# Kernel tuning notes

Hardware: AMD Instinct MI355X
Metric: run time of the kernel (lower is better)

Reference implementation:

```python
import jax, jax.numpy as jnp
import numpy as np

WEIGHT = 1.0

# 3x3x3 discrete Laplacian stencil (6-connected, center -6), as in the torch module
_LAP_K = jnp.array(
    [[[0, 0, 0], [0, 1, 0], [0, 0, 0]],
     [[0, 1, 0], [1, -6, 1], [0, 1, 0]],
     [[0, 0, 0], [0, 1, 0], [0, 0, 0]]], dtype=jnp.float32)


def _abs_laplacian3d(x):
    """x: (N, D, H, W) -> |3D Laplacian(x)| with zero padding, same shape."""
    y = jax.lax.conv_general_dilated(
        x[:, None],              # (N, 1, D, H, W)
        _LAP_K[None, None],      # (1, 1, 3, 3, 3)
        window_strides=(1, 1, 1),
        padding=[(1, 1), (1, 1), (1, 1)])
    return jnp.abs(y[:, 0])


def setup_inputs() -> dict:
    key = jax.random.key(0)
    k1, k2 = jax.random.split(key)
    B, C, D, H, W = 2, 4, 64, 256, 256
    logits = jax.random.normal(k1, (B, C, D, H, W), dtype=jnp.float32)
    targets = jax.random.randint(k2, (B, D, H, W), 0, C)
    return {"logits": logits, "targets": targets}


def reference(logits, targets):
    B, C, D, H, W = logits.shape
    # softmax over class dim, drop background class 0 -> (B, C-1, D, H, W)
    probs = jax.nn.softmax(logits, axis=1)[:, 1:]
    # one-hot target masks for classes 1..C-1 -> (B, C-1, D, H, W)
    cls = jnp.arange(1, C)[None, :, None, None, None]
    tmask = (targets[:, None] == cls).astype(logits.dtype)
    # fused 3D Laplacian + abs over all (batch, class) pairs at once
    pred_b = _abs_laplacian3d(probs.reshape(B * (C - 1), D, H, W))
    targ_b = _abs_laplacian3d(tmask.reshape(B * (C - 1), D, H, W))
    # sum over classes of per-class MSE, divided by (C-1) == mean over everything
    return WEIGHT * jnp.mean((pred_b - targ_b) ** 2)
```

## Files before the change

### kernel.cpp

```cpp
#include <hip/hip_runtime.h>


#define CS   (1 << 22)
#define NTOT_INV (1.0f / 25165824.0f)
#define BIAS3 ((8 << 20) | (8 << 10) | 8)
#define BAR() asm volatile("s_waitcnt lgkmcnt(0)\n\ts_barrier" ::: "memory")

#define ISSUE(S, off)                                                        \
    S##0 = *(const float4*)(L + lBase + (off));                              \
    S##1 = *(const float4*)(L + lBase + (off) + CS);                         \
    S##2 = *(const float4*)(L + lBase + (off) + 2 * CS);                     \
    S##3 = *(const float4*)(L + lBase + (off) + 3 * CS);                     \
    S##t = *(const int4*)(T + tBase + (off));

__device__ __forceinline__ void smax1(float x0, float x1, float x2, float x3,
                                      float vm, float& p1, float& p2, float& p3) {
    float e0 = __expf(x0);
    float e1 = __expf(x1);
    float e2 = __expf(x2);
    float e3 = __expf(x3);
    float r  = vm * __builtin_amdgcn_rcpf(e0 + e1 + e2 + e3);
    p1 = e1 * r; p2 = e2 * r; p3 = e3 * r;
}

__device__ __forceinline__ int ohenc(int t, int msk) {
    int nz = (t > 0) ? 1 : 0;
    return (nz << (((t - 1) & 3) * 10)) & msk;
}

__global__ __launch_bounds__(512) void boundary_loss_kernel(
        const float* __restrict__ L,
        const int*   __restrict__ T,
        float*       __restrict__ out) {
    const int tid  = threadIdx.x;
    const int lane = tid & 63;
    const int th   = tid >> 6;

    const int u  = blockIdx.x;
    int bi = (u & 7) * 86 + (u >> 3);
    const int dseg = bi & 7;  bi >>= 3;
    const int ht   = bi % 43;
    const int b    = bi / 43;

    const int   h   = ht * 6 + th - 1;
    const bool  hv  = ((unsigned)h < 256u);
    const int   hcl = min(max(h, 0), 255);
    const float vm  = hv ? 1.f : 0.f;
    const int   ohm = hv ? ~0 : 0;
    const bool  live = (th >= 1) && (th <= 6) && hv;
    const int   d0  = dseg << 3;

    const int rowoff = (hcl << 8) + (lane << 2);
    const int tBase  = b * CS + rowoff;
    const int lBase  = (b << 2) * CS + rowoff;

    __shared__ float P1[8][256], P2[8][256], P3[8][256];
    __shared__ int   OH[8][256];

    const int c0 = lane << 2;

    float4 c1, c2, c3; int4 coh;
    float4 a1, a2, a3; int4 aoh;
    float accv = 0.f;

    {
        const int   off  = (dseg > 0 ? d0 - 1 : 0) << 16;
        const float svm  = (dseg > 0) ? vm : 0.f;
        const int   sohm = (dseg > 0) ? ohm : 0;
        float4 q0, q1, q2, q3; int4 qt;
        ISSUE(q, off)
        smax1(q0.x, q1.x, q2.x, q3.x, svm, a1.x, a2.x, a3.x);
        smax1(q0.y, q1.y, q2.y, q3.y, svm, a1.y, a2.y, a3.y);
        smax1(q0.z, q1.z, q2.z, q3.z, svm, a1.z, a2.z, a3.z);
        smax1(q0.w, q1.w, q2.w, q3.w, svm, a1.w, a2.w, a3.w);
        aoh.x = ohenc(qt.x, sohm) + BIAS3; aoh.y = ohenc(qt.y, sohm) + BIAS3;
        aoh.z = ohenc(qt.z, sohm) + BIAS3; aoh.w = ohenc(qt.w, sohm) + BIAS3;
    }

    {
        const int off = d0 << 16;
        float4 q0, q1, q2, q3; int4 qt;
        ISSUE(q, off)
        smax1(q0.x, q1.x, q2.x, q3.x, vm, c1.x, c2.x, c3.x);
        smax1(q0.y, q1.y, q2.y, q3.y, vm, c1.y, c2.y, c3.y);
        smax1(q0.z, q1.z, q2.z, q3.z, vm, c1.z, c2.z, c3.z);
        smax1(q0.w, q1.w, q2.w, q3.w, vm, c1.w, c2.w, c3.w);
        coh.x = ohenc(qt.x, ohm); coh.y = ohenc(qt.y, ohm);
        coh.z = ohenc(qt.z, ohm); coh.w = ohenc(qt.w, ohm);
    }

    float4 A0, A1, A2, A3; int4 At;
    {
        const int off = (d0 + 1) << 16;
        ISSUE(A, off)
    }

#pragma unroll
    for (int i = 0; i < 8; ++i) {
        float4 B0, B1, B2, B3; int4 Bt;
        B0 = B1 = B2 = B3 = make_float4(0.f, 0.f, 0.f, 0.f);
        Bt = make_int4(0, 0, 0, 0);
        if (i < 7) {
            const int dn  = d0 + i + 2;
            const int off = (dn < 64 ? dn : 63) << 16;
            ISSUE(B, off)
        }

        BAR();
        *(float4*)&P1[th][c0] = c1;
        *(float4*)&P2[th][c0] = c2;
        *(float4*)&P3[th][c0] = c3;
        *(int4*)&OH[th][c0]   = coh;
        BAR();

        if (live) {
            float l1 = __shfl_up(c1.w, 1, 64);   float r1 = __shfl_down(c1.x, 1, 64);
            float l2 = __shfl_up(c2.w, 1, 64);   float r2 = __shfl_down(c2.x, 1, 64);
            float l3 = __shfl_up(c3.w, 1, 64);   float r3 = __shfl_down(c3.x, 1, 64);
            int   lo = __shfl_up(coh.w, 1, 64);  int   ro = __shfl_down(coh.x, 1, 64);
            if (lane == 0)  { l1 = l2 = l3 = 0.f; lo = 0; }
            if (lane == 63) { r1 = r2 = r3 = 0.f; ro = 0; }

            float4 uu, v;
            uu = *(float4*)&P1[th - 1][c0]; v = *(float4*)&P1[th + 1][c0];
            a1.x += uu.x + v.x + l1   + c1.y - 6.f * c1.x;
            a1.y += uu.y + v.y + c1.x + c1.z - 6.f * c1.y;
            a1.z += uu.z + v.z + c1.y + c1.w - 6.f * c1.z;
            a1.w += uu.w + v.w + c1.z + r1   - 6.f * c1.w;
            uu = *(float4*)&P2[th - 1][c0]; v = *(float4*)&P2[th + 1][c0];
            a2.x += uu.x + v.x + l2   + c2.y - 6.f * c2.x;
            a2.y += uu.y + v.y + c2.x + c2.z - 6.f * c2.y;
            a2.z += uu.z + v.z + c2.y + c2.w - 6.f * c2.z;
            a2.w += uu.w + v.w + c2.z + r2   - 6.f * c2.w;
            uu = *(float4*)&P3[th - 1][c0]; v = *(float4*)&P3[th + 1][c0];
            a3.x += uu.x + v.x + l3   + c3.y - 6.f * c3.x;
            a3.y += uu.y + v.y + c3.x + c3.z - 6.f * c3.y;
            a3.z += uu.z + v.z + c3.y + c3.w - 6.f * c3.z;
            a3.w += uu.w + v.w + c3.z + r3   - 6.f * c3.w;

            int4 iu = *(int4*)&OH[th - 1][c0];
            int4 id = *(int4*)&OH[th + 1][c0];
            aoh.x += iu.x + id.x + lo    + coh.y - 6 * coh.x;
            aoh.y += iu.y + id.y + coh.x + coh.z - 6 * coh.y;
            aoh.z += iu.z + id.z + coh.y + coh.w - 6 * coh.z;
            aoh.w += iu.w + id.w + coh.z + ro    - 6 * coh.w;
        }

        const int   dnA  = d0 + i + 1;
        const float vmn  = (dnA < 64) ? vm : 0.f;
        const int   ohmn = (dnA < 64) ? ohm : 0;
        float4 n1, n2, n3; int4 noh;
        smax1(A0.x, A1.x, A2.x, A3.x, vmn, n1.x, n2.x, n3.x);
        smax1(A0.y, A1.y, A2.y, A3.y, vmn, n1.y, n2.y, n3.y);
        smax1(A0.z, A1.z, A2.z, A3.z, vmn, n1.z, n2.z, n3.z);
        smax1(A0.w, A1.w, A2.w, A3.w, vmn, n1.w, n2.w, n3.w);
        noh.x = ohenc(At.x, ohmn); noh.y = ohenc(At.y, ohmn);
        noh.z = ohenc(At.z, ohmn); noh.w = ohenc(At.w, ohmn);

        if (live) {
            int t0 = aoh.x + noh.x, t1 = aoh.y + noh.y;
            int t2 = aoh.z + noh.z, t3 = aoh.w + noh.w;
            float lp, lt, df;
            lp = fabsf(a1.x + n1.x); lt = fabsf((float)((t0 & 1023) - 8));          df = lp - lt; accv = fmaf(df, df, accv);
            lp = fabsf(a2.x + n2.x); lt = fabsf((float)(((t0 >> 10) & 1023) - 8));  df = lp - lt; accv = fmaf(df, df, accv);
            lp = fabsf(a3.x + n3.x); lt = fabsf((float)(((t0 >> 20) & 1023) - 8));  df = lp - lt; accv = fmaf(df, df, accv);
            lp = fabsf(a1.y + n1.y); lt = fabsf((float)((t1 & 1023) - 8));          df = lp - lt; accv = fmaf(df, df, accv);
            lp = fabsf(a2.y + n2.y); lt = fabsf((float)(((t1 >> 10) & 1023) - 8));  df = lp - lt; accv = fmaf(df, df, accv);
            lp = fabsf(a3.y + n3.y); lt = fabsf((float)(((t1 >> 20) & 1023) - 8));  df = lp - lt; accv = fmaf(df, df, accv);
            lp = fabsf(a1.z + n1.z); lt = fabsf((float)((t2 & 1023) - 8));          df = lp - lt; accv = fmaf(df, df, accv);
            lp = fabsf(a2.z + n2.z); lt = fabsf((float)(((t2 >> 10) & 1023) - 8));  df = lp - lt; accv = fmaf(df, df, accv);
            lp = fabsf(a3.z + n3.z); lt = fabsf((float)(((t2 >> 20) & 1023) - 8));  df = lp - lt; accv = fmaf(df, df, accv);
            lp = fabsf(a1.w + n1.w); lt = fabsf((float)((t3 & 1023) - 8));          df = lp - lt; accv = fmaf(df, df, accv);
            lp = fabsf(a2.w + n2.w); lt = fabsf((float)(((t3 >> 10) & 1023) - 8));  df = lp - lt; accv = fmaf(df, df, accv);
            lp = fabsf(a3.w + n3.w); lt = fabsf((float)(((t3 >> 20) & 1023) - 8));  df = lp - lt; accv = fmaf(df, df, accv);
        }

        a1 = c1; a2 = c2; a3 = c3;
        aoh.x = coh.x + BIAS3; aoh.y = coh.y + BIAS3;
        aoh.z = coh.z + BIAS3; aoh.w = coh.w + BIAS3;
        c1 = n1; c2 = n2; c3 = n3; coh = noh;
        A0 = B0; A1 = B1; A2 = B2; A3 = B3; At = Bt;
    }

    for (int o = 32; o > 0; o >>= 1) accv += __shfl_down(accv, o, 64);
    __shared__ float wsum[8];
    if (lane == 0) wsum[th] = accv;
    __syncthreads();
    if (tid == 0) {
        float s = wsum[0] + wsum[1] + wsum[2] + wsum[3]
                + wsum[4] + wsum[5] + wsum[6] + wsum[7];
        atomicAdd(out, s * NTOT_INV);
    }
}

extern "C" void kernel_launch(void* const* d_in, const int* in_sizes, int n_in,
                              void* d_out, int out_size, void* d_ws, size_t ws_size,
                              hipStream_t stream) {
    const float* logits  = (const float*)d_in[0];
    const int*   targets = (const int*)d_in[1];
    float*       out     = (float*)d_out;

    hipMemsetAsync(out, 0, sizeof(float), stream);
    boundary_loss_kernel<<<688, 512, 0, stream>>>(logits, targets, out);
}
```

Baseline: 220.0 us.

## Replace LDS row sharing with per-thread halo row loads and recomputed softmax

Each wavefront now loads its own row plus the rows above and below straight from global memory and recomputes their softmax and one-hot encoding, rather than writing rows to LDS and sharing them across barriers. This removes the two block barriers per depth step and the halo warps that previously did no output work. Blocks become 256 threads and the grid grows to 1024. The cost is three times the global load traffic (mostly cache hits) and three times the exp and reciprocal work, plus more registers held by the triple prefetch.

```diff
diff --git a/kernel.cpp b/kernel.cpp
--- a/kernel.cpp
+++ b/kernel.cpp
@@ -4,14 +4,23 @@
 #define CS   (1 << 22)
 #define NTOT_INV (1.0f / 25165824.0f)
 #define BIAS3 ((8 << 20) | (8 << 10) | 8)
-#define BAR() asm volatile("s_waitcnt lgkmcnt(0)\n\ts_barrier" ::: "memory")
-
-#define ISSUE(S, off)                                                        \
-    S##0 = *(const float4*)(L + lBase + (off));                              \
-    S##1 = *(const float4*)(L + lBase + (off) + CS);                         \
-    S##2 = *(const float4*)(L + lBase + (off) + 2 * CS);                     \
-    S##3 = *(const float4*)(L + lBase + (off) + 3 * CS);                     \
-    S##t = *(const int4*)(T + tBase + (off));
+
+#define ISSUE3(off)                                                          \
+    Au0 = *(const float4*)(L + lBu + (off));                                 \
+    Au1 = *(const float4*)(L + lBu + (off) + CS);                            \
+    Au2 = *(const float4*)(L + lBu + (off) + 2 * CS);                        \
+    Au3 = *(const float4*)(L + lBu + (off) + 3 * CS);                        \
+    Aut = *(const int4*)(T + tBu + (off));                                   \
+    Ac0 = *(const float4*)(L + lBc + (off));                                 \
+    Ac1 = *(const float4*)(L + lBc + (off) + CS);                            \
+    Ac2 = *(const float4*)(L + lBc + (off) + 2 * CS);                        \
+    Ac3 = *(const float4*)(L + lBc + (off) + 3 * CS);                        \
+    Act = *(const int4*)(T + tBc + (off));                                   \
+    Ad0 = *(const float4*)(L + lBd + (off));                                 \
+    Ad1 = *(const float4*)(L + lBd + (off) + CS);                            \
+    Ad2 = *(const float4*)(L + lBd + (off) + 2 * CS);                        \
+    Ad3 = *(const float4*)(L + lBd + (off) + 3 * CS);                        \
+    Adt = *(const int4*)(T + tBd + (off));
 
 __device__ __forceinline__ void smax1(float x0, float x1, float x2, float x3,
                                       float vm, float& p1, float& p2, float& p3) {
@@ -28,7 +37,39 @@
     return (nz << (((t - 1) & 3) * 10)) & msk;
 }
 
-__global__ __launch_bounds__(512) void boundary_loss_kernel(
+#define COOK(P1, P2, P3, PO, R0, R1, R2, R3, RT, vmv, ohmv)                  \
+    smax1(R0.x, R1.x, R2.x, R3.x, vmv, P1.x, P2.x, P3.x);                    \
+    smax1(R0.y, R1.y, R2.y, R3.y, vmv, P1.y, P2.y, P3.y);                    \
+    smax1(R0.z, R1.z, R2.z, R3.z, vmv, P1.z, P2.z, P3.z);                    \
+    smax1(R0.w, R1.w, R2.w, R3.w, vmv, P1.w, P2.w, P3.w);                    \
+    PO.x = ohenc(RT.x, ohmv); PO.y = ohenc(RT.y, ohmv);                      \
+    PO.z = ohenc(RT.z, ohmv); PO.w = ohenc(RT.w, ohmv);
+
+#define TCOMP(TT, U, DN, N)                                                  \
+    {                                                                        \
+        float lft = __shfl_up(N.w, 1, 64);                                   \
+        float rgt = __shfl_down(N.x, 1, 64);                                 \
+        if (lane == 0)  lft = 0.f;                                           \
+        if (lane == 63) rgt = 0.f;                                           \
+        TT.x = U.x + DN.x + lft + N.y - 6.f * N.x;                           \
+        TT.y = U.y + DN.y + N.x + N.z - 6.f * N.y;                           \
+        TT.z = U.z + DN.z + N.y + N.w - 6.f * N.z;                           \
+        TT.w = U.w + DN.w + N.z + rgt - 6.f * N.w;                           \
+    }
+
+#define TCOMPI(TT, U, DN, N)                                                 \
+    {                                                                        \
+        int lft = __shfl_up(N.w, 1, 64);                                     \
+        int rgt = __shfl_down(N.x, 1, 64);                                   \
+        if (lane == 0)  lft = 0;                                             \
+        if (lane == 63) rgt = 0;                                             \
+        TT.x = U.x + DN.x + lft + N.y - 6 * N.x + BIAS3;                     \
+        TT.y = U.y + DN.y + N.x + N.z - 6 * N.y + BIAS3;                     \
+        TT.z = U.z + DN.z + N.y + N.w - 6 * N.z + BIAS3;                     \
+        TT.w = U.w + DN.w + N.z + rgt - 6 * N.w + BIAS3;                     \
+    }
+
+__global__ __launch_bounds__(256) void boundary_loss_kernel(
         const float* __restrict__ L,
         const int*   __restrict__ T,
         float*       __restrict__ out) {
@@ -37,158 +78,120 @@
     const int th   = tid >> 6;
 
     const int u  = blockIdx.x;
-    int bi = (u & 7) * 86 + (u >> 3);
-    const int dseg = bi & 7;  bi >>= 3;
-    const int ht   = bi % 43;
-    const int b    = bi / 43;
-
-    const int   h   = ht * 6 + th - 1;
-    const bool  hv  = ((unsigned)h < 256u);
-    const int   hcl = min(max(h, 0), 255);
-    const float vm  = hv ? 1.f : 0.f;
-    const int   ohm = hv ? ~0 : 0;
-    const bool  live = (th >= 1) && (th <= 6) && hv;
+    int bi = ((u & 7) << 7) | (u >> 3);
+    const int hq   = bi & 63;  bi >>= 6;
+    const int dseg = bi & 7;
+    const int b    = bi >> 3;
+
+    const int h  = hq * 4 + th;
+    const int hu = max(h - 1, 0);
+    const int hd = min(h + 1, 255);
+    const float vmu = (h > 0)   ? 1.f : 0.f;
+    const float vmd = (h < 255) ? 1.f : 0.f;
+    const int   omu = (h > 0)   ? ~0 : 0;
+    const int   omd = (h < 255) ? ~0 : 0;
     const int   d0  = dseg << 3;
 
-    const int rowoff = (hcl << 8) + (lane << 2);
-    const int tBase  = b * CS + rowoff;
-    const int lBase  = (b << 2) * CS + rowoff;
-
-    __shared__ float P1[8][256], P2[8][256], P3[8][256];
-    __shared__ int   OH[8][256];
-
-    const int c0 = lane << 2;
-
-    float4 c1, c2, c3; int4 coh;
-    float4 a1, a2, a3; int4 aoh;
+    const int lo  = lane << 2;
+    const int lBc = (b << 2) * CS + (h  << 8) + lo;
+    const int lBu = (b << 2) * CS + (hu << 8) + lo;
+    const int lBd = (b << 2) * CS + (hd << 8) + lo;
+    const int tBc = b * CS + (h  << 8) + lo;
+    const int tBu = b * CS + (hu << 8) + lo;
+    const int tBd = b * CS + (hd << 8) + lo;
+
+    float4 cp1, cp2, cp3; int4 cpo;
+    float4 c1,  c2,  c3;  int4 co;
+    float4 t1,  t2,  t3;  int4 to;
     float accv = 0.f;
 
+    float4 Au0, Au1, Au2, Au3; int4 Aut;
+    float4 Ac0, Ac1, Ac2, Ac3; int4 Act;
+    float4 Ad0, Ad1, Ad2, Ad3; int4 Adt;
+
     {
-        const int   off  = (dseg > 0 ? d0 - 1 : 0) << 16;
-        const float svm  = (dseg > 0) ? vm : 0.f;
-        const int   sohm = (dseg > 0) ? ohm : 0;
-        float4 q0, q1, q2, q3; int4 qt;
-        ISSUE(q, off)
-        smax1(q0.x, q1.x, q2.x, q3.x, svm, a1.x, a2.x, a3.x);
-        smax1(q0.y, q1.y, q2.y, q3.y, svm, a1.y, a2.y, a3.y);
-        smax1(q0.z, q1.z, q2.z, q3.z, svm, a1.z, a2.z, a3.z);
-        smax1(q0.w, q1.w, q2.w, q3.w, svm, a1.w, a2.w, a3.w);
-        aoh.x = ohenc(qt.x, sohm) + BIAS3; aoh.y = ohenc(qt.y, sohm) + BIAS3;
-        aoh.z = ohenc(qt.z, sohm) + BIAS3; aoh.w = ohenc(qt.w, sohm) + BIAS3;
+        const int   off = (dseg > 0 ? d0 - 1 : 0) << 16;
+        const float svm = (dseg > 0) ? 1.f : 0.f;
+        const int   som = (dseg > 0) ? ~0 : 0;
+        float4 q0 = *(const float4*)(L + lBc + off);
+        float4 q1 = *(const float4*)(L + lBc + off + CS);
+        float4 q2 = *(const float4*)(L + lBc + off + 2 * CS);
+        float4 q3 = *(const float4*)(L + lBc + off + 3 * CS);
+        int4   qt = *(const int4*)(T + tBc + off);
+        COOK(cp1, cp2, cp3, cpo, q0, q1, q2, q3, qt, svm, som)
     }
 
     {
-        const int off = d0 << 16;
-        float4 q0, q1, q2, q3; int4 qt;
-        ISSUE(q, off)
-        smax1(q0.x, q1.x, q2.x, q3.x, vm, c1.x, c2.x, c3.x);
-        smax1(q0.y, q1.y, q2.y, q3.y, vm, c1.y, c2.y, c3.y);
-        smax1(q0.z, q1.z, q2.z, q3.z, vm, c1.z, c2.z, c3.z);
-        smax1(q0.w, q1.w, q2.w, q3.w, vm, c1.w, c2.w, c3.w);
-        coh.x = ohenc(qt.x, ohm); coh.y = ohenc(qt.y, ohm);
-        coh.z = ohenc(qt.z, ohm); coh.w = ohenc(qt.w, ohm);
-    }
-
-    float4 A0, A1, A2, A3; int4 At;
-    {
-        const int off = (d0 + 1) << 16;
-        ISSUE(A, off)
-    }
-
-#pragma unroll
+        ISSUE3(d0 << 16)
+        float4 pu1, pu2, pu3; int4 puo;
+        float4 pd1, pd2, pd3; int4 pdo;
+        COOK(pu1, pu2, pu3, puo, Au0, Au1, Au2, Au3, Aut, vmu, omu)
+        COOK(pd1, pd2, pd3, pdo, Ad0, Ad1, Ad2, Ad3, Adt, vmd, omd)
+        COOK(c1,  c2,  c3,  co,  Ac0, Ac1, Ac2, Ac3, Act, 1.f, ~0)
+        TCOMP(t1, pu1, pd1, c1)
+        TCOMP(t2, pu2, pd2, c2)
+        TCOMP(t3, pu3, pd3, c3)
+        TCOMPI(to, puo, pdo, co)
+    }
+
+    ISSUE3((d0 + 1) << 16)
+
+#pragma unroll 2
     for (int i = 0; i < 8; ++i) {
-        float4 B0, B1, B2, B3; int4 Bt;
-        B0 = B1 = B2 = B3 = make_float4(0.f, 0.f, 0.f, 0.f);
-        Bt = make_int4(0, 0, 0, 0);
+        const int   pn  = d0 + i + 1;
+        const float vmp = (pn < 64) ? 1.f : 0.f;
+        const int   ohp = (pn < 64) ? ~0 : 0;
+
+        float4 pu1, pu2, pu3; int4 puo;
+        float4 pd1, pd2, pd3; int4 pdo;
+        float4 nc1, nc2, nc3; int4 nco;
+        COOK(pu1, pu2, pu3, puo, Au0, Au1, Au2, Au3, Aut, vmu * vmp, omu & ohp)
+        COOK(pd1, pd2, pd3, pdo, Ad0, Ad1, Ad2, Ad3, Adt, vmd * vmp, omd & ohp)
+        COOK(nc1, nc2, nc3, nco, Ac0, Ac1, Ac2, Ac3, Act, vmp,       ohp)
+
         if (i < 7) {
             const int dn  = d0 + i + 2;
             const int off = (dn < 64 ? dn : 63) << 16;
-            ISSUE(B, off)
+            ISSUE3(off)
         }
 
-        BAR();
-        *(float4*)&P1[th][c0] = c1;
-        *(float4*)&P2[th][c0] = c2;
-        *(float4*)&P3[th][c0] = c3;
-        *(int4*)&OH[th][c0]   = coh;
-        BAR();
-
-        if (live) {
-            float l1 = __shfl_up(c1.w, 1, 64);   float r1 = __shfl_down(c1.x, 1, 64);
-            float l2 = __shfl_up(c2.w, 1, 64);   float r2 = __shfl_down(c2.x, 1, 64);
-            float l3 = __shfl_up(c3.w, 1, 64);   float r3 = __shfl_down(c3.x, 1, 64);
-            int   lo = __shfl_up(coh.w, 1, 64);  int   ro = __shfl_down(coh.x, 1, 64);
-            if (lane == 0)  { l1 = l2 = l3 = 0.f; lo = 0; }
-            if (lane == 63) { r1 = r2 = r3 = 0.f; ro = 0; }
-
-            float4 uu, v;
-            uu = *(float4*)&P1[th - 1][c0]; v = *(float4*)&P1[th + 1][c0];
-            a1.x += uu.x + v.x + l1   + c1.y - 6.f * c1.x;
-            a1.y += uu.y + v.y + c1.x + c1.z - 6.f * c1.y;
-            a1.z += uu.z + v.z + c1.y + c1.w - 6.f * c1.z;
-            a1.w += uu.w + v.w + c1.z + r1   - 6.f * c1.w;
-            uu = *(float4*)&P2[th - 1][c0]; v = *(float4*)&P2[th + 1][c0];
-            a2.x += uu.x + v.x + l2   + c2.y - 6.f * c2.x;
-            a2.y += uu.y + v.y + c2.x + c2.z - 6.f * c2.y;
-            a2.z += uu.z + v.z + c2.y + c2.w - 6.f * c2.z;
-            a2.w += uu.w + v.w + c2.z + r2   - 6.f * c2.w;
-            uu = *(float4*)&P3[th - 1][c0]; v = *(float4*)&P3[th + 1][c0];
-            a3.x += uu.x + v.x + l3   + c3.y - 6.f * c3.x;
-            a3.y += uu.y + v.y + c3.x + c3.z - 6.f * c3.y;
-            a3.z += uu.z + v.z + c3.y + c3.w - 6.f * c3.z;
-            a3.w += uu.w + v.w + c3.z + r3   - 6.f * c3.w;
-
-            int4 iu = *(int4*)&OH[th - 1][c0];
-            int4 id = *(int4*)&OH[th + 1][c0];
-            aoh.x += iu.x + id.x + lo    + coh.y - 6 * coh.x;
-            aoh.y += iu.y + id.y + coh.x + coh.z - 6 * coh.y;
-            aoh.z += iu.z + id.z + coh.y + coh.w - 6 * coh.z;
-            aoh.w += iu.w + id.w + coh.z + ro    - 6 * coh.w;
+        float4 tn1, tn2, tn3; int4 tno;
+        TCOMP(tn1, pu1, pd1, nc1)
+        TCOMP(tn2, pu2, pd2, nc2)
+        TCOMP(tn3, pu3, pd3, nc3)
+        TCOMPI(tno, puo, pdo, nco)
+
+        {
+            int q0 = to.x + cpo.x + nco.x;
+            int q1 = to.y + cpo.y + nco.y;
+            int q2 = to.z + cpo.z + nco.z;
+            int q3 = to.w + cpo.w + nco.w;
+            float lp, lt, df;
+            lp = fabsf(t1.x + cp1.x + nc1.x); lt = fabsf((float)((q0 & 1023) - 8));          df = lp - lt; accv = fmaf(df, df, accv);
+            lp = fabsf(t2.x + cp2.x + nc2.x); lt = fabsf((float)(((q0 >> 10) & 1023) - 8));  df = lp - lt; accv = fmaf(df, df, accv);
+            lp = fabsf(t3.x + cp3.x + nc3.x); lt = fabsf((float)(((q0 >> 20) & 1023) - 8));  df = lp - lt; accv = fmaf(df, df, accv);
+            lp = fabsf(t1.y + cp1.y + nc1.y); lt = fabsf((float)((q1 & 1023) - 8));          df = lp - lt; accv = fmaf(df, df, accv);
+            lp = fabsf(t2.y + cp2.y + nc2.y); lt = fabsf((float)(((q1 >> 10) & 1023) - 8));  df = lp - lt; accv = fmaf(df, df, accv);
+            lp = fabsf(t3.y + cp3.y + nc3.y); lt = fabsf((float)(((q1 >> 20) & 1023) - 8));  df = lp - lt; accv = fmaf(df, df, accv);
+            lp = fabsf(t1.z + cp1.z + nc1.z); lt = fabsf((float)((q2 & 1023) - 8));          df = lp - lt; accv = fmaf(df, df, accv);
+            lp = fabsf(t2.z + cp2.z + nc2.z); lt = fabsf((float)(((q2 >> 10) & 1023) - 8));  df = lp - lt; accv = fmaf(df, df, accv);
+            lp = fabsf(t3.z + cp3.z + nc3.z); lt = fabsf((float)(((q2 >> 20) & 1023) - 8));  df = lp - lt; accv = fmaf(df, df, accv);
+            lp = fabsf(t1.w + cp1.w + nc1.w); lt = fabsf((float)((q3 & 1023) - 8));          df = lp - lt; accv = fmaf(df, df, accv);
+            lp = fabsf(t2.w + cp2.w + nc2.w); lt = fabsf((float)(((q3 >> 10) & 1023) - 8));  df = lp - lt; accv = fmaf(df, df, accv);
+            lp = fabsf(t3.w + cp3.w + nc3.w); lt = fabsf((float)(((q3 >> 20) & 1023) - 8));  df = lp - lt; accv = fmaf(df, df, accv);
         }
 
-        const int   dnA  = d0 + i + 1;
-        const float vmn  = (dnA < 64) ? vm : 0.f;
-        const int   ohmn = (dnA < 64) ? ohm : 0;
-        float4 n1, n2, n3; int4 noh;
-        smax1(A0.x, A1.x, A2.x, A3.x, vmn, n1.x, n2.x, n3.x);
-        smax1(A0.y, A1.y, A2.y, A3.y, vmn, n1.y, n2.y, n3.y);
-        smax1(A0.z, A1.z, A2.z, A3.z, vmn, n1.z, n2.z, n3.z);
-        smax1(A0.w, A1.w, A2.w, A3.w, vmn, n1.w, n2.w, n3.w);
-        noh.x = ohenc(At.x, ohmn); noh.y = ohenc(At.y, ohmn);
-        noh.z = ohenc(At.z, ohmn); noh.w = ohenc(At.w, ohmn);
-
-        if (live) {
-            int t0 = aoh.x + noh.x, t1 = aoh.y + noh.y;
-            int t2 = aoh.z + noh.z, t3 = aoh.w + noh.w;
-            float lp, lt, df;
-            lp = fabsf(a1.x + n1.x); lt = fabsf((float)((t0 & 1023) - 8));          df = lp - lt; accv = fmaf(df, df, accv);
-            lp = fabsf(a2.x + n2.x); lt = fabsf((float)(((t0 >> 10) & 1023) - 8));  df = lp - lt; accv = fmaf(df, df, accv);
-            lp = fabsf(a3.x + n3.x); lt = fabsf((float)(((t0 >> 20) & 1023) - 8));  df = lp - lt; accv = fmaf(df, df, accv);
-            lp = fabsf(a1.y + n1.y); lt = fabsf((float)((t1 & 1023) - 8));          df = lp - lt; accv = fmaf(df, df, accv);
-            lp = fabsf(a2.y + n2.y); lt = fabsf((float)(((t1 >> 10) & 1023) - 8));  df = lp - lt; accv = fmaf(df, df, accv);
-            lp = fabsf(a3.y + n3.y); lt = fabsf((float)(((t1 >> 20) & 1023) - 8));  df = lp - lt; accv = fmaf(df, df, accv);
-            lp = fabsf(a1.z + n1.z); lt = fabsf((float)((t2 & 1023) - 8));          df = lp - lt; accv = fmaf(df, df, accv);
-            lp = fabsf(a2.z + n2.z); lt = fabsf((float)(((t2 >> 10) & 1023) - 8));  df = lp - lt; accv = fmaf(df, df, accv);
-            lp = fabsf(a3.z + n3.z); lt = fabsf((float)(((t2 >> 20) & 1023) - 8));  df = lp - lt; accv = fmaf(df, df, accv);
-            lp = fabsf(a1.w + n1.w); lt = fabsf((float)((t3 & 1023) - 8));          df = lp - lt; accv = fmaf(df, df, accv);
-            lp = fabsf(a2.w + n2.w); lt = fabsf((float)(((t3 >> 10) & 1023) - 8));  df = lp - lt; accv = fmaf(df, df, accv);
-            lp = fabsf(a3.w + n3.w); lt = fabsf((float)(((t3 >> 20) & 1023) - 8));  df = lp - lt; accv = fmaf(df, df, accv);
-        }
-
-        a1 = c1; a2 = c2; a3 = c3;
-        aoh.x = coh.x + BIAS3; aoh.y = coh.y + BIAS3;
-        aoh.z = coh.z + BIAS3; aoh.w = coh.w + BIAS3;
-        c1 = n1; c2 = n2; c3 = n3; coh = noh;
-        A0 = B0; A1 = B1; A2 = B2; A3 = B3; At = Bt;
+        cp1 = c1; cp2 = c2; cp3 = c3; cpo = co;
+        c1 = nc1; c2 = nc2; c3 = nc3; co = nco;
+        t1 = tn1; t2 = tn2; t3 = tn3; to = tno;
     }
 
     for (int o = 32; o > 0; o >>= 1) accv += __shfl_down(accv, o, 64);
-    __shared__ float wsum[8];
+    __shared__ float wsum[4];
     if (lane == 0) wsum[th] = accv;
     __syncthreads();
     if (tid == 0) {
-        float s = wsum[0] + wsum[1] + wsum[2] + wsum[3]
-                + wsum[4] + wsum[5] + wsum[6] + wsum[7];
+        float s = wsum[0] + wsum[1] + wsum[2] + wsum[3];
         atomicAdd(out, s * NTOT_INV);
     }
 }
@@ -201,5 +204,5 @@
     float*       out     = (float*)d_out;
 
     hipMemsetAsync(out, 0, sizeof(float), stream);
-    boundary_loss_kernel<<<688, 512, 0, stream>>>(logits, targets, out);
-}
+    boundary_loss_kernel<<<1024, 256, 0, stream>>>(logits, targets, out);
+}
```

Result: slower. 243.7 us (+10.8%).
